# Performance work log

Measured on AMD Instinct MI355X. Metric: run time of the kernel, lower is better.

Reference implementation:

```python
import jax, jax.numpy as jnp
import numpy as np

# Fixed architecture constants from Cifar10Model / RetNetConfig
NL = 8            # num_layers
H = 4             # num_heads
D = 64            # hidden_size
QK = 64           # qk_dim
V = 128           # v_dim
QH, VH = QK // H, V // H   # 16, 32 per-head dims
P, IMG, C = 8, 32, 3       # patch size, image size, channels
NP = (IMG // P) ** 2       # 16 patches
T = NP + 1                 # +1 cls token -> 17 tokens
FFN = 12                   # ffn_proj_size


def layer_norm(x, s, b, eps=1e-5):
    mu = x.mean(-1, keepdims=True)
    var = x.var(-1, keepdims=True)
    return (x - mu) * jax.lax.rsqrt(var + eps) * s + b


def rotate_every_two(x):
    x1, x2 = x[..., ::2], x[..., 1::2]
    return jnp.stack([-x2, x1], axis=-1).reshape(x.shape)


def rel_pos(t):
    # xPos-style rotation angles over the per-head qk dim
    angle = 1.0 / (10000 ** jnp.linspace(0.0, 1.0, QH // 2))
    angle = jnp.repeat(angle, 2)                      # (QH,)
    idx = jnp.arange(t, dtype=jnp.float32)[:, None]
    sin, cos = jnp.sin(idx * angle), jnp.cos(idx * angle)   # (t, QH)
    # per-head retention decay gamma (use_default_gamma=False path)
    gamma = 1.0 - jnp.exp(jnp.linspace(np.log(1 / 32), np.log(1 / 512), H))  # (H,)
    n = jnp.arange(t)
    expo = n[:, None] - n[None, :]                    # n - m
    causal = expo >= 0
    dmask = jnp.where(causal, gamma[:, None, None] ** jnp.where(causal, expo, 0), 0.0)  # (H,t,t)
    dmask = dmask / jnp.sqrt(dmask.sum(-1, keepdims=True))   # row-normalized decay
    return sin, cos, dmask


def retention(x, Wq, Wk, Wv, Wg, Wo, sin, cos, dmask):
    b, t, _ = x.shape
    q = (x @ Wq).reshape(b, t, H, QH).transpose(0, 2, 1, 3)   # (b,h,t,qh)
    k = (x @ Wk).reshape(b, t, H, QH).transpose(0, 2, 1, 3)
    v = (x @ Wv).reshape(b, t, H, VH).transpose(0, 2, 1, 3)   # (b,h,t,vh)
    g = x @ Wg                                                # (b,t,V) gate
    q = q * cos + rotate_every_two(q) * sin
    k = (k * cos + rotate_every_two(k) * sin) * (QH ** -0.5)
    scores = jnp.einsum('bhnd,bhmd->bhnm', q, k) * dmask      # decay-masked QK^T
    denom = jnp.clip(jnp.abs(jax.lax.stop_gradient(scores).sum(-1, keepdims=True)), 1.0, None)
    scores = scores / denom                                   # retention row normalization
    o = jnp.einsum('bhnm,bhmd->bhnd', scores, v)              # (b,h,t,vh)
    # per-head group norm (no affine) instead of softmax normalization
    mu = o.mean(-1, keepdims=True)
    var = o.var(-1, keepdims=True)
    o = (o - mu) * jax.lax.rsqrt(var + 1e-5)
    o = o.transpose(0, 2, 1, 3).reshape(b, t, V)
    return (jax.nn.silu(g) * o) @ Wo


def setup_inputs() -> dict:
    key = jax.random.key(0)
    ks = iter(jax.random.split(key, 32))
    s = 0.02
    B = 8192
    inp = {
        'x': jax.random.normal(next(ks), (B, C, IMG, IMG), jnp.float32),
        'patch_w': jax.random.normal(next(ks), (C * P * P, D), jnp.float32) * s,
        'patch_b': jnp.zeros((D,), jnp.float32),
        'cls': jax.random.normal(next(ks), (1, 1, D), jnp.float32) * s,
        'pos': jax.random.normal(next(ks), (T, D), jnp.float32) * s,
        'Wq': jax.random.normal(next(ks), (NL, D, QK), jnp.float32) * s,
        'Wk': jax.random.normal(next(ks), (NL, D, QK), jnp.float32) * s,
        'Wv': jax.random.normal(next(ks), (NL, D, V), jnp.float32) * s,
        'Wg': jax.random.normal(next(ks), (NL, D, V), jnp.float32) * s,
        'Wo': jax.random.normal(next(ks), (NL, V, D), jnp.float32) * s,
        'ln1_s': jnp.ones((NL, D), jnp.float32),
        'ln1_b': jnp.zeros((NL, D), jnp.float32),
        'w1': jax.random.normal(next(ks), (NL, D, FFN), jnp.float32) * s,
        'b1': jnp.zeros((NL, FFN), jnp.float32),
        'w2': jax.random.normal(next(ks), (NL, FFN, D), jnp.float32) * s,
        'b2': jnp.zeros((NL, D), jnp.float32),
        'ln2_s': jnp.ones((NL, D), jnp.float32),
        'ln2_b': jnp.zeros((NL, D), jnp.float32),
        'lnf_s': jnp.ones((D,), jnp.float32),
        'lnf_b': jnp.zeros((D,), jnp.float32),
        'neck_w': jax.random.normal(next(ks), (D, 16), jnp.float32) * s,
        'neck_b': jnp.zeros((16,), jnp.float32),
        'head_w': jax.random.normal(next(ks), (16, 10), jnp.float32) * s,
        'head_b': jnp.zeros((10,), jnp.float32),
    }
    return inp


def reference(x, patch_w, patch_b, cls, pos, Wq, Wk, Wv, Wg, Wo, ln1_s, ln1_b,
              w1, b1, w2, b2, ln2_s, ln2_b, lnf_s, lnf_b, neck_w, neck_b, head_w, head_b):
    b = x.shape[0]
    # patch embedding: stride==kernel conv expressed as reshape + matmul
    xp = x.reshape(b, C, IMG // P, P, IMG // P, P).transpose(0, 2, 4, 1, 3, 5)
    xp = xp.reshape(b, NP, C * P * P)
    tok = xp @ patch_w + patch_b                          # (b,16,64)
    tok = jnp.concatenate([jnp.broadcast_to(cls, (b, 1, D)), tok], axis=1) + pos  # (b,17,64)
    sin, cos, dmask = rel_pos(T)
    h = tok
    for i in range(NL):  # pre-LN RetNet blocks
        h = h + retention(layer_norm(h, ln1_s[i], ln1_b[i]),
                          Wq[i], Wk[i], Wv[i], Wg[i], Wo[i], sin, cos, dmask)
        f = layer_norm(h, ln2_s[i], ln2_b[i])
        h = h + jax.nn.gelu(f @ w1[i] + b1[i]) @ w2[i] + b2[i]
    h = layer_norm(h, lnf_s, lnf_b)
    ys = h[:, -1, :]                                      # last token
    return (ys @ neck_w + neck_b) @ head_w + head_b       # (b,10) logits
```

## Files before the change

### kernel.cpp

```cpp
#include <hip/hip_runtime.h>
#include <hip/hip_bf16.h>

#define NLAY 8
#define MFMA __builtin_amdgcn_mfma_f32_16x16x32_bf16
#define MFMA32 __builtin_amdgcn_mfma_f32_32x32x16_bf16

typedef __attribute__((ext_vector_type(8))) short bf16x8;
typedef __attribute__((ext_vector_type(4))) float f32x4;
typedef __attribute__((ext_vector_type(16))) float f32x16;
typedef __attribute__((ext_vector_type(4))) int i32x4;

template <bool BF16>
__device__ __forceinline__ float ld(const void* p, int i) {
  if (BF16) {
    unsigned short u = ((const unsigned short*)p)[i];
    return __uint_as_float(((unsigned)u) << 16);
  }
  return ((const float*)p)[i];
}

template <bool BF16>
__device__ __forceinline__ float2 ld2(const void* p, int i) {
  float2 r;
  if (BF16) {
    unsigned u = ((const unsigned*)p)[i >> 1];
    r.x = __uint_as_float(u << 16);
    r.y = __uint_as_float(u & 0xffff0000u);
  } else {
    r = ((const float2*)p)[i >> 1];
  }
  return r;
}

__device__ __forceinline__ unsigned pack_bf2(float a, float b) {
  __hip_bfloat16 ha = __float2bfloat16(a), hb = __float2bfloat16(b);
  unsigned short ua, ub;
  __builtin_memcpy(&ua, &ha, 2);
  __builtin_memcpy(&ub, &hb, 2);
  return ((unsigned)ub << 16) | (unsigned)ua;
}

__device__ __forceinline__ unsigned short cvt_bf(float a) {
  __hip_bfloat16 h = __float2bfloat16(a);
  unsigned short us;
  __builtin_memcpy(&us, &h, 2);
  return us;
}

__device__ __forceinline__ float2 unpk(unsigned u) {
  float2 r;
  r.x = __uint_as_float(u << 16);
  r.y = __uint_as_float(u & 0xffff0000u);
  return r;
}

__device__ __forceinline__ bf16x8 as_bf(i32x4 v) {
  bf16x8 r;
  __builtin_memcpy(&r, &v, 16);
  return r;
}

template <bool BF16>
__device__ __forceinline__ void ld8v(const void* p, int i, float* v) {
  if (BF16) {
    i32x4 u = *(const i32x4*)((const unsigned short*)p + i);
    float2 a = unpk((unsigned)u.x); v[0] = a.x; v[1] = a.y;
    float2 b = unpk((unsigned)u.y); v[2] = b.x; v[3] = b.y;
    float2 c = unpk((unsigned)u.z); v[4] = c.x; v[5] = c.y;
    float2 d = unpk((unsigned)u.w); v[6] = d.x; v[7] = d.y;
  } else {
    float4 a = *(const float4*)((const float*)p + i);
    float4 b = *(const float4*)((const float*)p + i + 4);
    v[0] = a.x; v[1] = a.y; v[2] = a.z; v[3] = a.w;
    v[4] = b.x; v[5] = b.y; v[6] = b.z; v[7] = b.w;
  }
}

__global__ void setup_tables(float* __restrict__ ws, const void* __restrict__ x) {
  int tid = threadIdx.x;
  for (int idx = tid; idx < 272; idx += 256) {
    int t = idx >> 4, j = idx & 15;
    float a = powf(10000.f, -(float)(j >> 1) / 7.f);
    float arg = (float)t * a;
    ws[idx] = sinf(arg);
    ws[272 + idx] = cosf(arg);
  }
  for (int row = tid; row < 68; row += 256) {
    int hh = row / 17, t = row % 17;
    float gamma = 1.f - exp2f(-5.f - 4.f * (float)hh / 3.f);
    float sum = 0.f;
    for (int u = 0; u <= t; ++u) sum += powf(gamma, (float)(t - u));
    float rn = rsqrtf(sum);
    for (int u = 0; u < 17; ++u)
      ws[544 + row * 17 + u] = (u <= t) ? powf(gamma, (float)(t - u)) * rn : 0.f;
  }
  if (tid == 0) {
    const unsigned short* u16 = (const unsigned short*)x;
    int sane = 0;
    for (int i = 0; i < 128; ++i) {
      float v = __uint_as_float(((unsigned)u16[2 * i]) << 16);
      float av = fabsf(v);
      if (v == 0.f || (av > 1e-8f && av < 1e4f)) sane++;
    }
    ws[1700] = (sane >= 64) ? 1.f : 0.f;
  }
}

#define FRAG_OLD 280576
#define FRAG_TOT 305152
template <bool BF16>
__global__ void prep_frags(const void* __restrict__ patch_w,
                           const void* __restrict__ Wq, const void* __restrict__ Wk,
                           const void* __restrict__ Wv, const void* __restrict__ Wg,
                           const void* __restrict__ Wo, const void* __restrict__ w1,
                           const void* __restrict__ w2,
                           const float* __restrict__ tab,
                           unsigned short* __restrict__ frag) {
  if ((tab[1700] > 0.5f) != BF16) return;
  int g = blockIdx.x * 256 + threadIdx.x;
  if (g >= FRAG_TOT) return;
  float v;
  if (g < 12288) {
    int nt = g / 3072, r = g % 3072, kt = r / 512, r2 = r % 512, la = r2 >> 3, j = r2 & 7;
    int n = nt * 16 + (la & 15), k = kt * 32 + (la >> 4) * 8 + j;
    v = ld<BF16>(patch_w, k * 64 + n);
  } else if (g < FRAG_OLD) {
    int gg = g - 12288, l = gg / 33536, o = gg % 33536;
    if (o < 8192) {
      const void* W = (o < 4096) ? Wq : Wk;
      int e = o & 4095;
      int nt = e / 1024, r = e % 1024, kt = r / 512, r2 = r % 512, la = r2 >> 3, j = r2 & 7;
      int n = nt * 16 + (la & 15), k = kt * 32 + (la >> 4) * 8 + j;
      v = ld<BF16>(W, l * 4096 + k * 64 + n);
    } else if (o < 24576) {
      const void* W = (o < 16384) ? Wv : Wg;
      int e = (o - 8192) & 8191;
      int nt = e / 1024, r = e % 1024, kt = r / 512, r2 = r % 512, la = r2 >> 3, j = r2 & 7;
      int n = nt * 16 + (la & 15), k = kt * 32 + (la >> 4) * 8 + j;
      v = ld<BF16>(W, l * 8192 + k * 128 + n);
    } else if (o < 32768) {
      int e = o - 24576;
      int nt = e / 2048, r = e % 2048, kt = r / 512, r2 = r % 512, la = r2 >> 3, j = r2 & 7;
      int n = nt * 16 + (la & 15), k = kt * 32 + (la >> 4) * 8 + j;
      v = ld<BF16>(Wo, l * 8192 + k * 64 + n);
    } else {
      int e = o - 32768, eo = e / 64, d = e % 64;
      v = ld<BF16>(w1, l * 768 + d * 12 + eo);
    }
  } else {
    int gg = g - FRAG_OLD, l = gg / 3072, o = gg % 3072;
    if (o < 1024) {
      int kt = o >> 9, r = o & 511, la = r >> 3, j = r & 7;
      int n = la & 15, k = kt * 32 + (la >> 4) * 8 + j;
      v = (n < 12) ? ld<BF16>(w1, l * 768 + k * 12 + n) : 0.f;
    } else {
      int e2 = o - 1024;
      int nt = e2 >> 9, r = e2 & 511, la = r >> 3, j = r & 7;
      int n = nt * 16 + (la & 15), k = (la >> 4) * 8 + j;
      v = (k < 12) ? ld<BF16>(w2, (l * 12 + k) * 64 + n) : 0.f;
    }
  }
  __hip_bfloat16 h = __float2bfloat16(v);
  unsigned short us;
  __builtin_memcpy(&us, &h, 2);
  frag[g] = us;
}

#define O_DM   0
#define O_SIN  1156
#define O_COS  1428
#define O_ST   1700
#define O_H    2212
#define O_XNF  4456
#define O_FF   5992
#define O_R    6400
#define O_SCA  11024
#define O_VG   14096
#define SM_TOT 18968

template <bool BF16>
__global__ void __launch_bounds__(512, 4)
vit_fused(const void* __restrict__ x, const void* __restrict__ patch_b,
          const void* __restrict__ cls, const void* __restrict__ pos,
          const void* __restrict__ ln1s, const void* __restrict__ ln1b,
          const void* __restrict__ b1, const void* __restrict__ b2,
          const void* __restrict__ ln2s, const void* __restrict__ ln2b,
          const void* __restrict__ lnfs, const void* __restrict__ lnfb,
          const void* __restrict__ neckw, const void* __restrict__ neckb,
          const void* __restrict__ headw, const void* __restrict__ headb,
          const float* __restrict__ tab, const unsigned short* __restrict__ FR,
          void* __restrict__ out) {
  if ((tab[1700] > 0.5f) != BF16) return;

  const int tid = threadIdx.x;
  const int lane = tid & 63, w = tid >> 6;
  const int lq = lane >> 4, ln = lane & 15;
  const int img0 = 2 * blockIdx.x;

  __shared__ __align__(16) float sm[SM_TOT];
  float* sDM  = sm + O_DM;
  float* sSin = sm + O_SIN;
  float* sCos = sm + O_COS;
  float* sST  = sm + O_ST;
  float* sH   = sm + O_H;
  float* sFF  = sm + O_FF;
  unsigned short* sQb = (unsigned short*)(sm + O_R);
  unsigned short* sKb = ((unsigned short*)(sm + O_R)) + 2312;
  float* sO   = sm + O_R;
  unsigned short* sVbT = (unsigned short*)(sm + O_VG);
  unsigned short* sGb  = (unsigned short*)(sm + O_VG) + 5120;
  const bf16x8* FRB = (const bf16x8*)FR;

  for (int i = tid; i < 1156; i += 512) sDM[i] = tab[544 + i] * 0.25f;
  for (int i = tid; i < 272; i += 512) { sSin[i] = tab[i]; sCos[i] = tab[272 + i]; }
  for (int s = tid; s < 768; s += 512) {
    int mt = s / 384, r = s % 384, kt = r / 64, la = r % 64;
    int p = la & 15, q = la >> 4;
    int kb = kt * 32 + q * 8;
    int c = kb >> 6, rem = kb & 63, a = rem >> 3;
    int pi = p >> 2, pj = p & 3;
    int src = (img0 + mt) * 3072 + c * 1024 + (pi * 8 + a) * 32 + pj * 8;
    float v[8];
#pragma unroll
    for (int t2 = 0; t2 < 8; t2 += 2) {
      float2 pv = ld2<BF16>(x, src + t2);
      v[t2] = pv.x; v[t2 + 1] = pv.y;
    }
    i32x4 pk;
    pk.x = pack_bf2(v[0], v[1]); pk.y = pack_bf2(v[2], v[3]);
    pk.z = pack_bf2(v[4], v[5]); pk.w = pack_bf2(v[6], v[7]);
    ((i32x4*)(sm + O_SCA))[s] = pk;
  }
  if (tid < 128) {
    int img = tid >> 6, n = tid & 63;
    sH[(img * 17) * 66 + n] = ld<BF16>(cls, n) + ld<BF16>(pos, n);
  }
  __syncthreads();

  {
    int mt = w >> 2, nt = w & 3;
    f32x4 acc = {0.f, 0.f, 0.f, 0.f};
    const bf16x8* paf = (const bf16x8*)(sm + O_SCA);
#pragma unroll
    for (int kt = 0; kt < 6; ++kt)
      acc = MFMA(paf[(mt * 6 + kt) * 64 + lane], FRB[(nt * 6 + kt) * 64 + lane], acc, 0, 0, 0);
    int n = nt * 16 + ln;
    float pb = ld<BF16>(patch_b, n);
#pragma unroll
    for (int i = 0; i < 4; ++i) {
      int t = 1 + lq * 4 + i;
      sH[(mt * 17 + t) * 66 + n] = acc[i] + pb + ld<BF16>(pos, t * 64 + n);
    }
  }
  __syncthreads();

  for (int l = 0; l < NLAY; ++l) {
    const int LB = 1536 + l * 4192;

    if (tid < 320) {
      int la = tid & 63, wv = tid >> 6;
      int m = wv * 8 + (la & 7);
      int sub = ((la >> 3) & 3) + 4 * (la >> 5);
      i32x4 pk = {0, 0, 0, 0};
      if (m < 34) {
        const float2* hp = (const float2*)(sH + m * 66 + sub * 8);
        float2 h0 = hp[0], h1 = hp[1], h2 = hp[2], h3 = hp[3];
        float s1 = 0.f, s2 = 0.f;
        s1 += h0.x; s2 += h0.x * h0.x; s1 += h0.y; s2 += h0.y * h0.y;
        s1 += h1.x; s2 += h1.x * h1.x; s1 += h1.y; s2 += h1.y * h1.y;
        s1 += h2.x; s2 += h2.x * h2.x; s1 += h2.y; s2 += h2.y * h2.y;
        s1 += h3.x; s2 += h3.x * h3.x; s1 += h3.y; s2 += h3.y * h3.y;
        s1 += __shfl_xor(s1, 8);  s2 += __shfl_xor(s2, 8);
        s1 += __shfl_xor(s1, 16); s2 += __shfl_xor(s2, 16);
        s1 += __shfl_xor(s1, 32); s2 += __shfl_xor(s2, 32);
        float mu = s1 * (1.f / 64.f);
        float var = s2 * (1.f / 64.f) - mu * mu;
        float rr = rsqrtf(var + 1e-5f);
        int kb = sub * 8;
        float hv[8] = {h0.x, h0.y, h1.x, h1.y, h2.x, h2.y, h3.x, h3.y};
        float sv[8], bv[8];
        ld8v<BF16>(ln1s, l * 64 + kb, sv);
        ld8v<BF16>(ln1b, l * 64 + kb, bv);
        float vv[8];
#pragma unroll
        for (int t2 = 0; t2 < 8; ++t2)
          vv[t2] = (hv[t2] - mu) * rr * sv[t2] + bv[t2];
        pk.x = pack_bf2(vv[0], vv[1]); pk.y = pack_bf2(vv[2], vv[3]);
        pk.z = pack_bf2(vv[4], vv[5]); pk.w = pack_bf2(vv[6], vv[7]);
      }
      int slot = (m >> 4) * 128 + (sub >> 2) * 64 + (sub & 3) * 16 + (m & 15);
      ((i32x4*)(sm + O_XNF))[slot] = pk;
    }
    __syncthreads();

    {
      const bf16x8* xnf = (const bf16x8*)(sm + O_XNF);
      {
        const bf16x8* wf = FRB + LB + ((w < 4) ? 0 : 512);
        unsigned short* dst = (w < 4) ? sQb : sKb;
        int ntl = w & 3;
        int n = ntl * 16 + ln;
        int j0 = n & 14;
        float sgn = (n & 1) ? 1.f : -1.f;
#pragma unroll
        for (int mt = 0; mt < 3; ++mt) {
          f32x4 acc = {0.f, 0.f, 0.f, 0.f};
          acc = MFMA(xnf[(mt * 2) * 64 + lane], wf[(ntl * 2) * 64 + lane], acc, 0, 0, 0);
          acc = MFMA(xnf[(mt * 2 + 1) * 64 + lane], wf[(ntl * 2 + 1) * 64 + lane], acc, 0, 0, 0);
          unsigned short rbf[4];
#pragma unroll
          for (int i = 0; i < 4; ++i) {
            float part = __shfl_xor(acc[i], 1);
            int t = lq * 4 + i - mt;
            if (t < 0) t += 17;
            float cv = sCos[t * 16 + j0], sv = sSin[t * 16 + j0];
            rbf[i] = cvt_bf(acc[i] * cv + part * (sgn * sv));
          }
          if (mt < 2) {
            unsigned short* p = dst + (mt * 16 + lq * 4) * 68 + n;
            p[0] = rbf[0]; p[68] = rbf[1]; p[136] = rbf[2]; p[204] = rbf[3];
          } else if (lq == 0) {
            unsigned short* p = dst + 32 * 68 + n;
            p[0] = rbf[0]; p[68] = rbf[1];
          }
        }
      }
      {
        const bf16x8* wf = FRB + LB + 1024;
        int n = w * 16 + ln;
#pragma unroll
        for (int mt = 0; mt < 3; ++mt) {
          f32x4 acc = {0.f, 0.f, 0.f, 0.f};
          acc = MFMA(xnf[(mt * 2) * 64 + lane], wf[(w * 2) * 64 + lane], acc, 0, 0, 0);
          acc = MFMA(xnf[(mt * 2 + 1) * 64 + lane], wf[(w * 2 + 1) * 64 + lane], acc, 0, 0, 0);
          if (mt == 0) {
            uint2 uv;
            uv.x = pack_bf2(acc[0], acc[1]);
            uv.y = pack_bf2(acc[2], acc[3]);
            *(uint2*)(sVbT + n * 20 + lq * 4) = uv;
          } else if (mt == 1) {
#pragma unroll
            for (int i = 0; i < 4; ++i) {
              int m = 16 + lq * 4 + i;
              int img = (m >= 17), t = m - img * 17;
              sVbT[img * 2560 + n * 20 + t] = cvt_bf(acc[i]);
            }
          } else if (lq == 0) {
            sVbT[2560 + n * 20 + 15] = cvt_bf(acc[0]);
            sVbT[2560 + n * 20 + 16] = cvt_bf(acc[1]);
          }
        }
      }
      {
        const bf16x8* wf = FRB + LB + 2048;
        int n = w * 16 + ln;
#pragma unroll
        for (int mt = 0; mt < 3; ++mt) {
          f32x4 acc = {0.f, 0.f, 0.f, 0.f};
          acc = MFMA(xnf[(mt * 2) * 64 + lane], wf[(w * 2) * 64 + lane], acc, 0, 0, 0);
          acc = MFMA(xnf[(mt * 2 + 1) * 64 + lane], wf[(w * 2 + 1) * 64 + lane], acc, 0, 0, 0);
          if (mt < 2) {
            unsigned short* p = sGb + (mt * 16 + lq * 4) * 136 + n;
            p[0] = cvt_bf(acc[0]); p[136] = cvt_bf(acc[1]);
            p[272] = cvt_bf(acc[2]); p[408] = cvt_bf(acc[3]);
          } else if (lq == 0) {
            sGb[32 * 136 + n] = cvt_bf(acc[0]);
            sGb[33 * 136 + n] = cvt_bf(acc[1]);
          }
        }
      }
    }
    __syncthreads();

    {
      int img = w >> 2, hh = w & 3;
      int cl = lane & 31, kh = lane >> 5;
      int tt = (cl < 17) ? cl : 16;
      int m = img * 17 + tt;
      int off = m * 68 + hh * 16 + kh * 8;
      const uint2* qr = (const uint2*)(sQb + off);
      uint2 q0 = qr[0], q1 = qr[1];
      const uint2* kr = (const uint2*)(sKb + off);
      uint2 k0 = kr[0], k1 = kr[1];
      i32x4 ap; ap.x = (int)q0.x; ap.y = (int)q0.y; ap.z = (int)q1.x; ap.w = (int)q1.y;
      i32x4 bp; bp.x = (int)k0.x; bp.y = (int)k0.y; bp.z = (int)k1.x; bp.w = (int)k1.y;
      const unsigned short* vcol = sVbT + img * 2560 + (hh * 32 + cl) * 20 + kh * 8;
      uint2 v0 = ((const uint2*)vcol)[0], v1 = ((const uint2*)vcol)[1];
      i32x4 bpv; bpv.x = (int)v0.x; bpv.y = (int)v0.y; bpv.z = (int)v1.x; bpv.w = (int)v1.y;
      unsigned short v16 = sVbT[img * 2560 + (hh * 32 + cl) * 20 + 16];
      __syncthreads();

      f32x16 acc = {0.f, 0.f, 0.f, 0.f, 0.f, 0.f, 0.f, 0.f,
                    0.f, 0.f, 0.f, 0.f, 0.f, 0.f, 0.f, 0.f};
      acc = MFMA32(as_bf(bp), as_bf(ap), acc, 0, 0, 0);
      const float* dmr = sDM + hh * 289 + tt * 17;
      float p[16];
#pragma unroll
      for (int r = 0; r < 16; ++r) {
        int u = (r & 3) + 8 * (r >> 2) + 4 * kh;
        p[r] = (u <= 16) ? acc[r] * dmr[u] : 0.f;
      }
      float own = 0.f;
#pragma unroll
      for (int r = 0; r < 16; ++r) own += p[r];
      float den = fabsf(own + __shfl_xor(own, 32));
      if (den < 1.f) den = 1.f;
      den = __builtin_amdgcn_rcpf(den);
      float ex[4];
#pragma unroll
      for (int j = 0; j < 4; ++j)
        ex[j] = __shfl_xor((kh == 0) ? p[4 + j] : p[j], 32);
      float pd[8];
#pragma unroll
      for (int j = 0; j < 4; ++j) {
        pd[j]     = ((kh == 0) ? p[j]  : ex[j])     * den;
        pd[4 + j] = ((kh == 0) ? ex[j] : p[4 + j])  * den;
      }
      i32x4 apv;
      apv.x = pack_bf2(pd[0], pd[1]); apv.y = pack_bf2(pd[2], pd[3]);
      apv.z = pack_bf2(pd[4], pd[5]); apv.w = pack_bf2(pd[6], pd[7]);
      f32x16 ao = {0.f, 0.f, 0.f, 0.f, 0.f, 0.f, 0.f, 0.f,
                   0.f, 0.f, 0.f, 0.f, 0.f, 0.f, 0.f, 0.f};
      ao = MFMA32(as_bf(apv), as_bf(bpv), ao, 0, 0, 0);
      i32x4 a1 = {0, 0, 0, 0}, b1v = {0, 0, 0, 0};
      if (kh == 0) {
        a1.x = (int)(unsigned)cvt_bf(p[8] * den);
        b1v.x = (int)(unsigned)v16;
      }
      ao = MFMA32(as_bf(a1), as_bf(b1v), ao, 0, 0, 0);
      int cg = hh * 32 + cl;
#pragma unroll
      for (int r = 0; r < 16; ++r) {
        int t = (r & 3) + 8 * (r >> 2) + 4 * kh;
        if (t < 17) sO[(img * 17 + t) * 134 + cg] = ao[r];
      }
    }
    __syncthreads();

    for (int s = tid; s < 768; s += 512) {
      int mt = s >> 8, kt = (s >> 6) & 3, la = s & 63;
      int q = la >> 4, m = mt * 16 + (la & 15);
      int cb = kt * 32 + q * 8;
      i32x4 pk = {0, 0, 0, 0};
      if (m < 34) {
        const float2* op = (const float2*)(sO + m * 134 + cb);
        float2 o0 = op[0], o1 = op[1], o2 = op[2], o3 = op[3];
        float s1 = 0.f, s2 = 0.f;
        s1 += o0.x; s2 += o0.x * o0.x; s1 += o0.y; s2 += o0.y * o0.y;
        s1 += o1.x; s2 += o1.x * o1.x; s1 += o1.y; s2 += o1.y * o1.y;
        s1 += o2.x; s2 += o2.x * o2.x; s1 += o2.y; s2 += o2.y * o2.y;
        s1 += o3.x; s2 += o3.x * o3.x; s1 += o3.y; s2 += o3.y * o3.y;
        s1 += __shfl_xor(s1, 16); s2 += __shfl_xor(s2, 16);
        s1 += __shfl_xor(s1, 32); s2 += __shfl_xor(s2, 32);
        float mu = s1 * (1.f / 32.f);
        float var = s2 * (1.f / 32.f) - mu * mu;
        float rr = rsqrtf(var + 1e-5f);
        i32x4 gu = *(const i32x4*)(sGb + m * 136 + cb);
        float ov[8] = {o0.x, o0.y, o1.x, o1.y, o2.x, o2.y, o3.x, o3.y};
        float vv[8];
#pragma unroll
        for (int q2 = 0; q2 < 4; ++q2) {
          unsigned gw = (q2 == 0) ? (unsigned)gu.x : (q2 == 1) ? (unsigned)gu.y
                       : (q2 == 2) ? (unsigned)gu.z : (unsigned)gu.w;
          float2 gv = unpk(gw);
          float on0 = (ov[2 * q2] - mu) * rr;
          float on1 = (ov[2 * q2 + 1] - mu) * rr;
          vv[2 * q2]     = on0 * gv.x * __builtin_amdgcn_rcpf(1.f + __expf(-gv.x));
          vv[2 * q2 + 1] = on1 * gv.y * __builtin_amdgcn_rcpf(1.f + __expf(-gv.y));
        }
        pk.x = pack_bf2(vv[0], vv[1]); pk.y = pack_bf2(vv[2], vv[3]);
        pk.z = pack_bf2(vv[4], vv[5]); pk.w = pack_bf2(vv[6], vv[7]);
      }
      ((i32x4*)(sm + O_SCA))[s] = pk;
    }
    __syncthreads();

    {
      const bf16x8* oaf = (const bf16x8*)(sm + O_SCA);
      const bf16x8* wof = FRB + LB + 3072;
      for (int j = w; j < 12; j += 8) {
        int mt = j >> 2, nt = j & 3;
        f32x4 acc = {0.f, 0.f, 0.f, 0.f};
#pragma unroll
        for (int kt = 0; kt < 4; ++kt)
          acc = MFMA(oaf[(mt * 4 + kt) * 64 + lane], wof[(nt * 4 + kt) * 64 + lane], acc, 0, 0, 0);
        int n = nt * 16 + ln;
#pragma unroll
        for (int i = 0; i < 4; ++i) {
          int m = mt * 16 + lq * 4 + i;
          if (m < 34) sH[m * 66 + n] += acc[i];
        }
      }
    }
    __syncthreads();

    if (tid < 320) {
      int la = tid & 63, wv = tid >> 6;
      int m = wv * 8 + (la & 7);
      int sub = ((la >> 3) & 3) + 4 * (la >> 5);
      i32x4 pk = {0, 0, 0, 0};
      if (m < 34) {
        const float2* hp = (const float2*)(sH + m * 66 + sub * 8);
        float2 h0 = hp[0], h1 = hp[1], h2 = hp[2], h3 = hp[3];
        float s1 = 0.f, s2 = 0.f;
        s1 += h0.x; s2 += h0.x * h0.x; s1 += h0.y; s2 += h0.y * h0.y;
        s1 += h1.x; s2 += h1.x * h1.x; s1 += h1.y; s2 += h1.y * h1.y;
        s1 += h2.x; s2 += h2.x * h2.x; s1 += h2.y; s2 += h2.y * h2.y;
        s1 += h3.x; s2 += h3.x * h3.x; s1 += h3.y; s2 += h3.y * h3.y;
        s1 += __shfl_xor(s1, 8);  s2 += __shfl_xor(s2, 8);
        s1 += __shfl_xor(s1, 16); s2 += __shfl_xor(s2, 16);
        s1 += __shfl_xor(s1, 32); s2 += __shfl_xor(s2, 32);
        float mu = s1 * (1.f / 64.f);
        float var = s2 * (1.f / 64.f) - mu * mu;
        float rr = rsqrtf(var + 1e-5f);
        int kb = sub * 8;
        float hv[8] = {h0.x, h0.y, h1.x, h1.y, h2.x, h2.y, h3.x, h3.y};
        float sv[8], bv[8];
        ld8v<BF16>(ln2s, l * 64 + kb, sv);
        ld8v<BF16>(ln2b, l * 64 + kb, bv);
        float vv[8];
#pragma unroll
        for (int t2 = 0; t2 < 8; ++t2)
          vv[t2] = (hv[t2] - mu) * rr * sv[t2] + bv[t2];
        pk.x = pack_bf2(vv[0], vv[1]); pk.y = pack_bf2(vv[2], vv[3]);
        pk.z = pack_bf2(vv[4], vv[5]); pk.w = pack_bf2(vv[6], vv[7]);
      }
      int slot = (m >> 4) * 128 + (sub >> 2) * 64 + (sub & 3) * 16 + (m & 15);
      ((i32x4*)(sm + O_XNF))[slot] = pk;
    }
    __syncthreads();

    if (w < 3) {
      const bf16x8* xnf = (const bf16x8*)(sm + O_XNF);
      const bf16x8* w1f = FRB + 35072 + l * 384;
      int mt = w;
      f32x4 acc = {0.f, 0.f, 0.f, 0.f};
#pragma unroll
      for (int kt = 0; kt < 2; ++kt)
        acc = MFMA(xnf[(mt * 2 + kt) * 64 + lane], w1f[kt * 64 + lane], acc, 0, 0, 0);
      if (ln < 12) {
        float b = ld<BF16>(b1, l * 12 + ln);
#pragma unroll
        for (int i = 0; i < 4; ++i) {
          int m = mt * 16 + lq * 4 + i;
          if (m < 34) {
            float a = acc[i] + b;
            float inner = 0.7978845608028654f * (a + 0.044715f * a * a * a);
            float e = __expf(2.f * inner);
            float th = 1.f - 2.f * __builtin_amdgcn_rcpf(e + 1.f);
            sFF[m * 12 + ln] = 0.5f * a * (1.f + th);
          }
        }
      }
    }
    __syncthreads();

    {
      const bf16x8* w2f = FRB + 35072 + l * 384 + 128;
      for (int j = w; j < 12; j += 8) {
        int mt = j >> 2, nt = j & 3;
        i32x4 ap = {0, 0, 0, 0};
        int ma = mt * 16 + ln;
        if (ma < 34) {
          const float4* fp4 = (const float4*)(sFF + ma * 12);
          if (lq == 0) {
            float4 a = fp4[0], b4 = fp4[1];
            ap.x = pack_bf2(a.x, a.y); ap.y = pack_bf2(a.z, a.w);
            ap.z = pack_bf2(b4.x, b4.y); ap.w = pack_bf2(b4.z, b4.w);
          } else if (lq == 1) {
            float4 c4 = fp4[2];
            ap.x = pack_bf2(c4.x, c4.y); ap.y = pack_bf2(c4.z, c4.w);
          }
        }
        f32x4 acc = {0.f, 0.f, 0.f, 0.f};
        acc = MFMA(as_bf(ap), w2f[nt * 64 + lane], acc, 0, 0, 0);
        int n = nt * 16 + ln;
        float b = ld<BF16>(b2, l * 64 + n);
#pragma unroll
        for (int i = 0; i < 4; ++i) {
          int m = mt * 16 + lq * 4 + i;
          if (m < 34) sH[m * 66 + n] += acc[i] + b;
        }
      }
    }
    __syncthreads();
  }

  if (tid < 2) {
    int m = tid * 17 + 16;
    float s1 = 0.f, s2 = 0.f;
    for (int d = 0; d < 64; ++d) {
      float v = sH[m * 66 + d];
      s1 += v; s2 += v * v;
    }
    float mu = s1 * (1.f / 64.f);
    float var = s2 * (1.f / 64.f) - mu * mu;
    sST[tid] = mu;
    sST[2 + tid] = rsqrtf(var + 1e-5f);
  }
  __syncthreads();
  if (tid < 32) {
    int img = tid >> 4, jn = tid & 15;
    int m = img * 17 + 16;
    float mu = sST[img], rr = sST[2 + img];
    float acc = ld<BF16>(neckb, jn);
    for (int d = 0; d < 64; ++d) {
      float yn = (sH[m * 66 + d] - mu) * rr * ld<BF16>(lnfs, d) + ld<BF16>(lnfb, d);
      acc += yn * ld<BF16>(neckw, d * 16 + jn);
    }
    sST[8 + img * 16 + jn] = acc;
  }
  __syncthreads();
  if (tid < 20) {
    int img = tid / 10, o = tid % 10;
    float acc = ld<BF16>(headb, o);
#pragma unroll
    for (int e = 0; e < 16; ++e) acc += sST[8 + img * 16 + e] * ld<BF16>(headw, e * 10 + o);
    if (BF16) {
      ((__hip_bfloat16*)out)[(img0 + img) * 10 + o] = __float2bfloat16(acc);
    } else {
      ((float*)out)[(img0 + img) * 10 + o] = acc;
    }
  }
}

extern "C" void kernel_launch(void* const* d_in, const int* in_sizes, int n_in,
                              void* d_out, int out_size, void* d_ws, size_t ws_size,
                              hipStream_t stream) {
  float* tab = (float*)d_ws;
  unsigned short* frag = (unsigned short*)((char*)d_ws + 8192);

  setup_tables<<<dim3(1), dim3(256), 0, stream>>>(tab, d_in[0]);

  const int prepBlocks = (FRAG_TOT + 255) / 256;
  prep_frags<false><<<dim3(prepBlocks), dim3(256), 0, stream>>>(
      d_in[1], d_in[5], d_in[6], d_in[7], d_in[8], d_in[9], d_in[12], d_in[14], tab, frag);
  prep_frags<true><<<dim3(prepBlocks), dim3(256), 0, stream>>>(
      d_in[1], d_in[5], d_in[6], d_in[7], d_in[8], d_in[9], d_in[12], d_in[14], tab, frag);

  const int B = in_sizes[0] / 3072;
  const int grid = B / 2;

  vit_fused<false><<<dim3(grid), dim3(512), 0, stream>>>(
      d_in[0], d_in[2], d_in[3], d_in[4], d_in[10], d_in[11], d_in[13],
      d_in[15], d_in[16], d_in[17], d_in[18], d_in[19], d_in[20], d_in[21],
      d_in[22], d_in[23], tab, frag, d_out);
  vit_fused<true><<<dim3(grid), dim3(512), 0, stream>>>(
      d_in[0], d_in[2], d_in[3], d_in[4], d_in[10], d_in[11], d_in[13],
      d_in[15], d_in[16], d_in[17], d_in[18], d_in[19], d_in[20], d_in[21],
      d_in[22], d_in[23], tab, frag, d_out);
}
```

Baseline: 727.3 us.

## Fuse LN2, FFN up and down projections per wave and cut block barriers

Merges the LN2 normalization, the FFN first matmul with GELU, and the FFN second matmul into one three-wave section. Each wave handles its own 16-row tile with wave-local LDS communication instead of block-wide __syncthreads, which removes two barriers per layer. It also stores the retention output as bf16 in a different LDS region, which halves those LDS writes and reads. It drops the barrier after the Q/K/V register loads, relying on the new buffer placement so that in-flight reads are not overwritten. The risks are wave-level LDS ordering hazards, since only an s_waitcnt and a compiler fence protect them, plus a small precision loss from storing the output in bf16.

```diff
diff --git a/kernel.cpp b/kernel.cpp
--- a/kernel.cpp
+++ b/kernel.cpp
@@ -206,7 +206,7 @@
   float* sFF  = sm + O_FF;
   unsigned short* sQb = (unsigned short*)(sm + O_R);
   unsigned short* sKb = ((unsigned short*)(sm + O_R)) + 2312;
-  float* sO   = sm + O_R;
+  unsigned short* sOb = (unsigned short*)(sm + O_SCA);
   unsigned short* sVbT = (unsigned short*)(sm + O_VG);
   unsigned short* sGb  = (unsigned short*)(sm + O_VG) + 5120;
   const bf16x8* FRB = (const bf16x8*)FR;
@@ -388,7 +388,6 @@
       uint2 v0 = ((const uint2*)vcol)[0], v1 = ((const uint2*)vcol)[1];
       i32x4 bpv; bpv.x = (int)v0.x; bpv.y = (int)v0.y; bpv.z = (int)v1.x; bpv.w = (int)v1.y;
       unsigned short v16 = sVbT[img * 2560 + (hh * 32 + cl) * 20 + 16];
-      __syncthreads();
 
       f32x16 acc = {0.f, 0.f, 0.f, 0.f, 0.f, 0.f, 0.f, 0.f,
                     0.f, 0.f, 0.f, 0.f, 0.f, 0.f, 0.f, 0.f};
@@ -432,7 +431,7 @@
 #pragma unroll
       for (int r = 0; r < 16; ++r) {
         int t = (r & 3) + 8 * (r >> 2) + 4 * kh;
-        if (t < 17) sO[(img * 17 + t) * 134 + cg] = ao[r];
+        if (t < 17) sOb[(img * 17 + t) * 140 + cg] = cvt_bf(ao[r]);
       }
     }
     __syncthreads();
@@ -443,8 +442,9 @@
       int cb = kt * 32 + q * 8;
       i32x4 pk = {0, 0, 0, 0};
       if (m < 34) {
-        const float2* op = (const float2*)(sO + m * 134 + cb);
-        float2 o0 = op[0], o1 = op[1], o2 = op[2], o3 = op[3];
+        const uint2* op2 = (const uint2*)(sOb + m * 140 + cb);
+        uint2 oa = op2[0], obv = op2[1];
+        float2 o0 = unpk(oa.x), o1 = unpk(oa.y), o2 = unpk(obv.x), o3 = unpk(obv.y);
         float s1 = 0.f, s2 = 0.f;
         s1 += o0.x; s2 += o0.x * o0.x; s1 += o0.y; s2 += o0.y * o0.y;
         s1 += o1.x; s2 += o1.x * o1.x; s1 += o1.y; s2 += o1.y * o1.y;
@@ -471,12 +471,12 @@
         pk.x = pack_bf2(vv[0], vv[1]); pk.y = pack_bf2(vv[2], vv[3]);
         pk.z = pack_bf2(vv[4], vv[5]); pk.w = pack_bf2(vv[6], vv[7]);
       }
-      ((i32x4*)(sm + O_SCA))[s] = pk;
+      ((i32x4*)(sm + O_R))[s] = pk;
     }
     __syncthreads();
 
     {
-      const bf16x8* oaf = (const bf16x8*)(sm + O_SCA);
+      const bf16x8* oaf = (const bf16x8*)(sm + O_R);
       const bf16x8* wof = FRB + LB + 3072;
       for (int j = w; j < 12; j += 8) {
         int mt = j >> 2, nt = j & 3;
@@ -494,92 +494,96 @@
     }
     __syncthreads();
 
-    if (tid < 320) {
-      int la = tid & 63, wv = tid >> 6;
-      int m = wv * 8 + (la & 7);
-      int sub = ((la >> 3) & 3) + 4 * (la >> 5);
-      i32x4 pk = {0, 0, 0, 0};
-      if (m < 34) {
-        const float2* hp = (const float2*)(sH + m * 66 + sub * 8);
-        float2 h0 = hp[0], h1 = hp[1], h2 = hp[2], h3 = hp[3];
-        float s1 = 0.f, s2 = 0.f;
-        s1 += h0.x; s2 += h0.x * h0.x; s1 += h0.y; s2 += h0.y * h0.y;
-        s1 += h1.x; s2 += h1.x * h1.x; s1 += h1.y; s2 += h1.y * h1.y;
-        s1 += h2.x; s2 += h2.x * h2.x; s1 += h2.y; s2 += h2.y * h2.y;
-        s1 += h3.x; s2 += h3.x * h3.x; s1 += h3.y; s2 += h3.y * h3.y;
-        s1 += __shfl_xor(s1, 8);  s2 += __shfl_xor(s2, 8);
-        s1 += __shfl_xor(s1, 16); s2 += __shfl_xor(s2, 16);
-        s1 += __shfl_xor(s1, 32); s2 += __shfl_xor(s2, 32);
-        float mu = s1 * (1.f / 64.f);
-        float var = s2 * (1.f / 64.f) - mu * mu;
-        float rr = rsqrtf(var + 1e-5f);
-        int kb = sub * 8;
-        float hv[8] = {h0.x, h0.y, h1.x, h1.y, h2.x, h2.y, h3.x, h3.y};
-        float sv[8], bv[8];
-        ld8v<BF16>(ln2s, l * 64 + kb, sv);
-        ld8v<BF16>(ln2b, l * 64 + kb, bv);
-        float vv[8];
-#pragma unroll
-        for (int t2 = 0; t2 < 8; ++t2)
-          vv[t2] = (hv[t2] - mu) * rr * sv[t2] + bv[t2];
-        pk.x = pack_bf2(vv[0], vv[1]); pk.y = pack_bf2(vv[2], vv[3]);
-        pk.z = pack_bf2(vv[4], vv[5]); pk.w = pack_bf2(vv[6], vv[7]);
-      }
-      int slot = (m >> 4) * 128 + (sub >> 2) * 64 + (sub & 3) * 16 + (m & 15);
-      ((i32x4*)(sm + O_XNF))[slot] = pk;
-    }
-    __syncthreads();
-
     if (w < 3) {
-      const bf16x8* xnf = (const bf16x8*)(sm + O_XNF);
+#pragma unroll
+      for (int pass = 0; pass < 2; ++pass) {
+        int m = w * 16 + pass * 8 + (lane >> 3);
+        int sub = lane & 7;
+        if (m < 34) {
+          const float2* hp = (const float2*)(sH + m * 66 + sub * 8);
+          float2 h0 = hp[0], h1 = hp[1], h2 = hp[2], h3 = hp[3];
+          float s1 = 0.f, s2 = 0.f;
+          s1 += h0.x; s2 += h0.x * h0.x; s1 += h0.y; s2 += h0.y * h0.y;
+          s1 += h1.x; s2 += h1.x * h1.x; s1 += h1.y; s2 += h1.y * h1.y;
+          s1 += h2.x; s2 += h2.x * h2.x; s1 += h2.y; s2 += h2.y * h2.y;
+          s1 += h3.x; s2 += h3.x * h3.x; s1 += h3.y; s2 += h3.y * h3.y;
+          s1 += __shfl_xor(s1, 1); s2 += __shfl_xor(s2, 1);
+          s1 += __shfl_xor(s1, 2); s2 += __shfl_xor(s2, 2);
+          s1 += __shfl_xor(s1, 4); s2 += __shfl_xor(s2, 4);
+          if (sub == 0) {
+            float mu = s1 * (1.f / 64.f);
+            float var = s2 * (1.f / 64.f) - mu * mu;
+            sST[m] = mu;
+            sST[34 + m] = rsqrtf(var + 1e-5f);
+          }
+        }
+      }
+      asm volatile("s_waitcnt lgkmcnt(0)" ::: "memory");
+      int mA = w * 16 + ln;
+      i32x4 pkf[2];
+#pragma unroll
+      for (int kt = 0; kt < 2; ++kt) {
+        int kb = kt * 32 + lq * 8;
+        i32x4 pkk = {0, 0, 0, 0};
+        if (mA < 34) {
+          float mu = sST[mA], rr = sST[34 + mA];
+          const float2* hp = (const float2*)(sH + mA * 66 + kb);
+          float2 h0 = hp[0], h1 = hp[1], h2 = hp[2], h3 = hp[3];
+          float hv[8] = {h0.x, h0.y, h1.x, h1.y, h2.x, h2.y, h3.x, h3.y};
+          float sv[8], bv[8];
+          ld8v<BF16>(ln2s, l * 64 + kb, sv);
+          ld8v<BF16>(ln2b, l * 64 + kb, bv);
+          float vv[8];
+#pragma unroll
+          for (int t2 = 0; t2 < 8; ++t2)
+            vv[t2] = (hv[t2] - mu) * rr * sv[t2] + bv[t2];
+          pkk.x = pack_bf2(vv[0], vv[1]); pkk.y = pack_bf2(vv[2], vv[3]);
+          pkk.z = pack_bf2(vv[4], vv[5]); pkk.w = pack_bf2(vv[6], vv[7]);
+        }
+        pkf[kt] = pkk;
+      }
       const bf16x8* w1f = FRB + 35072 + l * 384;
-      int mt = w;
       f32x4 acc = {0.f, 0.f, 0.f, 0.f};
-#pragma unroll
-      for (int kt = 0; kt < 2; ++kt)
-        acc = MFMA(xnf[(mt * 2 + kt) * 64 + lane], w1f[kt * 64 + lane], acc, 0, 0, 0);
+      acc = MFMA(as_bf(pkf[0]), w1f[lane], acc, 0, 0, 0);
+      acc = MFMA(as_bf(pkf[1]), w1f[64 + lane], acc, 0, 0, 0);
       if (ln < 12) {
         float b = ld<BF16>(b1, l * 12 + ln);
 #pragma unroll
         for (int i = 0; i < 4; ++i) {
-          int m = mt * 16 + lq * 4 + i;
-          if (m < 34) {
+          int mr = w * 16 + lq * 4 + i;
+          if (mr < 34) {
             float a = acc[i] + b;
             float inner = 0.7978845608028654f * (a + 0.044715f * a * a * a);
             float e = __expf(2.f * inner);
             float th = 1.f - 2.f * __builtin_amdgcn_rcpf(e + 1.f);
-            sFF[m * 12 + ln] = 0.5f * a * (1.f + th);
+            sFF[mr * 12 + ln] = 0.5f * a * (1.f + th);
           }
         }
       }
-    }
-    __syncthreads();
-
-    {
+      asm volatile("" ::: "memory");
+      i32x4 apf = {0, 0, 0, 0};
+      if (mA < 34) {
+        const float4* fp4 = (const float4*)(sFF + mA * 12);
+        if (lq == 0) {
+          float4 a = fp4[0], b4 = fp4[1];
+          apf.x = pack_bf2(a.x, a.y); apf.y = pack_bf2(a.z, a.w);
+          apf.z = pack_bf2(b4.x, b4.y); apf.w = pack_bf2(b4.z, b4.w);
+        } else if (lq == 1) {
+          float4 c4 = fp4[2];
+          apf.x = pack_bf2(c4.x, c4.y); apf.y = pack_bf2(c4.z, c4.w);
+        }
+      }
       const bf16x8* w2f = FRB + 35072 + l * 384 + 128;
-      for (int j = w; j < 12; j += 8) {
-        int mt = j >> 2, nt = j & 3;
-        i32x4 ap = {0, 0, 0, 0};
-        int ma = mt * 16 + ln;
-        if (ma < 34) {
-          const float4* fp4 = (const float4*)(sFF + ma * 12);
-          if (lq == 0) {
-            float4 a = fp4[0], b4 = fp4[1];
-            ap.x = pack_bf2(a.x, a.y); ap.y = pack_bf2(a.z, a.w);
-            ap.z = pack_bf2(b4.x, b4.y); ap.w = pack_bf2(b4.z, b4.w);
-          } else if (lq == 1) {
-            float4 c4 = fp4[2];
-            ap.x = pack_bf2(c4.x, c4.y); ap.y = pack_bf2(c4.z, c4.w);
-          }
-        }
-        f32x4 acc = {0.f, 0.f, 0.f, 0.f};
-        acc = MFMA(as_bf(ap), w2f[nt * 64 + lane], acc, 0, 0, 0);
+#pragma unroll
+      for (int nt = 0; nt < 4; ++nt) {
+        f32x4 a2 = {0.f, 0.f, 0.f, 0.f};
+        a2 = MFMA(as_bf(apf), w2f[nt * 64 + lane], a2, 0, 0, 0);
         int n = nt * 16 + ln;
         float b = ld<BF16>(b2, l * 64 + n);
 #pragma unroll
         for (int i = 0; i < 4; ++i) {
-          int m = mt * 16 + lq * 4 + i;
-          if (m < 34) sH[m * 66 + n] += acc[i] + b;
+          int m2 = w * 16 + lq * 4 + i;
+          if (m2 < 34) sH[m2 * 66 + n] += a2[i] + b;
         }
       }
     }
```

Measured after the change: 768.1 us. 5.6% more time.
